# Performance work log

Measured on AMD Instinct MI355X. Metric: run time of the kernel, lower is better.

Reference implementation:

```python
import jax, jax.numpy as jnp
import numpy as np

B, S, D, H = 2, 2048, 2048, 16
DK = D // H


def setup_inputs() -> dict:
    key = jax.random.key(0)
    k1, k2, k3 = jax.random.split(key, 3)
    x = jax.random.normal(k1, (B, S, D), dtype=jnp.float32)
    # trunc-normal in the original; plain normal with matching std is fine for a numeric baseline
    std_qkv = 2.0 / (DK + D)  # note: original passes variance as std to trunc_normal_
    W_qkv = jax.random.normal(k2, (3 * D, D), dtype=jnp.float32) * std_qkv
    W_o = jax.random.normal(k3, (D, D), dtype=jnp.float32) * (1.0 / D)
    return {"x": x, "W_qkv": W_qkv, "W_o": W_o}


def reference(x, W_qkv, W_o):
    b, s, d = x.shape
    # fused QKV projection: y = x @ W_qkv^T
    qkv = jnp.einsum('bsd,ed->bse', x, W_qkv)  # [b, s, 3d]
    q, k, v = jnp.split(qkv, 3, axis=-1)
    # [b, s, d] -> [b, h, s, dk]
    def to_heads(t):
        return t.reshape(b, s, H, DK).transpose(0, 2, 1, 3)
    q, k, v = to_heads(q), to_heads(k), to_heads(v)
    scores = jnp.einsum('bhqd,bhkd->bhqk', q, k) / np.sqrt(DK).astype(np.float32)
    causal = jnp.tril(jnp.ones((s, s), dtype=bool))
    scores = jnp.where(causal, scores, -jnp.inf)
    att = jax.nn.softmax(scores, axis=-1)
    out = jnp.einsum('bhqk,bhkd->bhqd', att, v)  # [b, h, s, dk]
    out = out.transpose(0, 2, 1, 3).reshape(b, s, d)
    return jnp.einsum('bsd,od->bso', out, W_o)
```

## Files before the change

### kernel.cpp

```cpp
#include <hip/hip_runtime.h>

typedef _Float16 f16;
typedef _Float16 f16x4 __attribute__((ext_vector_type(4)));
typedef _Float16 f16x8 __attribute__((ext_vector_type(8)));
typedef float    f32x4 __attribute__((ext_vector_type(4)));

#define MFMA_F16(a,b,c) __builtin_amdgcn_mfma_f32_16x16x32_f16((a),(b),(c),0,0,0)

static constexpr int B_  = 2;
static constexpr int S_  = 2048;
static constexpr int D_  = 2048;
static constexpr int H_  = 16;
static constexpr int DK_ = 128;
static constexpr int K_  = 2048;

__device__ __forceinline__ void gload_lds16(const void* g, void* l) {
  __builtin_amdgcn_global_load_lds(
      (const __attribute__((address_space(1))) void*)g,
      (__attribute__((address_space(3))) void*)l, 16, 0, 0);
}

__global__ __launch_bounds__(256) void cast_f16_kernel(const float* __restrict__ in,
                                                       f16* __restrict__ out, int n4) {
  int i = blockIdx.x * 256 + threadIdx.x;
  int stride = gridDim.x * 256;
  for (int j = i; j < n4; j += stride) {
    float4 v = reinterpret_cast<const float4*>(in)[j];
    f16x4 o = {(f16)v.x, (f16)v.y, (f16)v.z, (f16)v.w};
    reinterpret_cast<f16x4*>(out)[j] = o;
  }
}

__device__ __forceinline__ void gemm_core(const f16* __restrict__ A, const f16* __restrict__ Bw,
                                          int brow, int bcol, f16* As, f16* Bs,
                                          f32x4 (&acc)[4][4]) {
  const int tid = threadIdx.x;
  const int w = tid >> 6, l = tid & 63;
  const int lg = l >> 4, lr = l & 15;
  const int wr = w >> 1, wc = w & 1;
#pragma unroll
  for (int mi = 0; mi < 4; ++mi)
#pragma unroll
    for (int ni = 0; ni < 4; ++ni) acc[mi][ni] = (f32x4){0.f, 0.f, 0.f, 0.f};

  const int rA = brow * 128 + (l >> 2);
  const int rB = bcol * 128 + (l >> 2);
  const int ck = (l & 3) * 8;

  for (int kt = 0; kt < K_ / 32; ++kt) {
    __syncthreads();
#pragma unroll
    for (int i = 0; i < 2; ++i) {
      const int c = w + i * 4;
      gload_lds16(A  + (size_t)(rA + c * 16) * K_ + kt * 32 + ck, As + c * 512);
      gload_lds16(Bw + (size_t)(rB + c * 16) * K_ + kt * 32 + ck, Bs + c * 512);
    }
    __syncthreads();
    f16x8 af[4], bf[4];
#pragma unroll
    for (int mi = 0; mi < 4; ++mi)
      af[mi] = *(const f16x8*)(As + (wr * 64 + mi * 16 + lr) * 32 + lg * 8);
#pragma unroll
    for (int ni = 0; ni < 4; ++ni)
      bf[ni] = *(const f16x8*)(Bs + (wc * 64 + ni * 16 + lr) * 32 + lg * 8);
#pragma unroll
    for (int mi = 0; mi < 4; ++mi)
#pragma unroll
      for (int ni = 0; ni < 4; ++ni)
        acc[mi][ni] = MFMA_F16(af[mi], bf[ni], acc[mi][ni]);
  }
}

__global__ __launch_bounds__(256) void gemm_qkv_kernel(const f16* __restrict__ xb,
                                                       const f16* __restrict__ wqkv,
                                                       f16* __restrict__ Q,
                                                       f16* __restrict__ Kk,
                                                       f16* __restrict__ V) {
  __shared__ __align__(16) f16 As[4096];
  __shared__ __align__(16) f16 Bs[4096];
  const int bid = blockIdx.x;
  const int swz = (bid & 7) * (1536 / 8) + (bid >> 3);
  const int brow = swz / 48, bcol = swz % 48;

  f32x4 acc[4][4];
  gemm_core(xb, wqkv, brow, bcol, As, Bs, acc);

  const int tid = threadIdx.x;
  const int w = tid >> 6, l = tid & 63;
  const int lg = l >> 4, lr = l & 15;
  const int wr = w >> 1, wc = w & 1;

  const int which = bcol / 16;
  const int h = bcol % 16;
  f16* outp = (which == 0) ? Q : ((which == 1) ? Kk : V);
  const float scale = (which == 0) ? 0.08838834764831845f : 1.0f;

#pragma unroll
  for (int mi = 0; mi < 4; ++mi) {
    const int mbase = brow * 128 + wr * 64 + mi * 16 + lg * 4;
#pragma unroll
    for (int ni = 0; ni < 4; ++ni) {
      const int dk = wc * 64 + ni * 16 + lr;
#pragma unroll
      for (int r = 0; r < 4; ++r) {
        const int mm = mbase + r;
        const int b = mm >> 11, s = mm & 2047;
        outp[(((size_t)b * H_ + h) * S_ + s) * DK_ + dk] = (f16)(acc[mi][ni][r] * scale);
      }
    }
  }
}

__global__ __launch_bounds__(256) void gemm_out_kernel(const f16* __restrict__ ab,
                                                       const f16* __restrict__ wo,
                                                       float* __restrict__ out) {
  __shared__ __align__(16) f16 As[4096];
  __shared__ __align__(16) f16 Bs[4096];
  const int bid = blockIdx.x;
  const int swz = (bid & 7) * (512 / 8) + (bid >> 3);
  const int brow = swz / 16, bcol = swz % 16;

  f32x4 acc[4][4];
  gemm_core(ab, wo, brow, bcol, As, Bs, acc);

  const int tid = threadIdx.x;
  const int w = tid >> 6, l = tid & 63;
  const int lg = l >> 4, lr = l & 15;
  const int wr = w >> 1, wc = w & 1;

#pragma unroll
  for (int mi = 0; mi < 4; ++mi) {
    const int mbase = brow * 128 + wr * 64 + mi * 16 + lg * 4;
#pragma unroll
    for (int ni = 0; ni < 4; ++ni) {
      const int n = bcol * 128 + wc * 64 + ni * 16 + lr;
#pragma unroll
      for (int r = 0; r < 4; ++r)
        out[(size_t)(mbase + r) * D_ + n] = acc[mi][ni][r];
    }
  }
}

__global__ __launch_bounds__(256) void transpose_v_kernel(const f16* __restrict__ V,
                                                          f16* __restrict__ Vt) {
  const int bid = blockIdx.x;
  const int dt = bid & 1;
  const int st = (bid >> 1) & 31;
  const int bh = bid >> 6;
  __shared__ __align__(16) f16 t[64][72];
  const int tid = threadIdx.x;
#pragma unroll
  for (int i = 0; i < 2; ++i) {
    const int chunk = i * 256 + tid;
    const int row = chunk >> 3, c8 = chunk & 7;
    f16x8 v = *(const f16x8*)(V + ((size_t)bh * S_ + st * 64 + row) * DK_ + dt * 64 + c8 * 8);
    *(f16x8*)&t[row][c8 * 8] = v;
  }
  __syncthreads();
#pragma unroll
  for (int i = 0; i < 2; ++i) {
    const int chunk = i * 256 + tid;
    const int row = chunk >> 3, c8 = chunk & 7;
    f16x8 v;
#pragma unroll
    for (int jj = 0; jj < 8; ++jj) v[jj] = t[c8 * 8 + jj][row];
    *(f16x8*)(Vt + ((size_t)bh * DK_ + dt * 64 + row) * S_ + st * 64 + c8 * 8) = v;
  }
}

__global__ __launch_bounds__(256) void attn_kernel(const f16* __restrict__ Q,
                                                   const f16* __restrict__ Kg,
                                                   const f16* __restrict__ Vt,
                                                   f16* __restrict__ O) {
  __shared__ __align__(16) unsigned char Ks[64 * 256];
  __shared__ __align__(16) unsigned char Vs[128 * 128];
  __shared__ __align__(16) unsigned char Ps[4][16 * 128];

  const int bid = blockIdx.x;
  const int pr = bid & 15;
  const int h  = (bid >> 4) & 15;
  const int b  = bid >> 8;
  const int bh = b * H_ + h;
  const int tid = threadIdx.x;
  const int w = tid >> 6, l = tid & 63;
  const int lg = l >> 4, lr = l & 15;

  for (int half = 0; half < 2; ++half) {
    const int qt = half ? (31 - pr) : pr;

    const f16* Qg = Q + ((size_t)bh * S_ + qt * 64 + w * 16) * DK_;
    f16x8 qf[4];
#pragma unroll
    for (int kd = 0; kd < 4; ++kd)
      qf[kd] = *(const f16x8*)(Qg + (size_t)lr * DK_ + kd * 32 + lg * 8);

    f32x4 o[8];
#pragma unroll
    for (int n = 0; n < 8; ++n) o[n] = (f32x4){0.f, 0.f, 0.f, 0.f};
    float mrun[4] = {-1e30f, -1e30f, -1e30f, -1e30f};
    float lrun[4] = {0.f, 0.f, 0.f, 0.f};

    const int ntiles = qt + 1;
    for (int kt = 0; kt < ntiles; ++kt) {
      __syncthreads();
      const f16* Kt = Kg + ((size_t)bh * S_ + kt * 64) * DK_;
#pragma unroll
      for (int i = 0; i < 4; ++i) {
        const int chunk = i * 256 + tid;
        const int row = chunk >> 4, c8 = chunk & 15;
        uint4 v = *(const uint4*)(Kt + (size_t)row * DK_ + c8 * 8);
        *(uint4*)(Ks + row * 256 + ((c8 * 16) ^ ((row & 7) << 4))) = v;
      }
      const f16* Vtt = Vt + (size_t)bh * DK_ * S_ + kt * 64;
#pragma unroll
      for (int i = 0; i < 4; ++i) {
        const int chunk = i * 256 + tid;
        const int row = chunk >> 3, c8 = chunk & 7;
        uint4 v = *(const uint4*)(Vtt + (size_t)row * S_ + c8 * 8);
        *(uint4*)(Vs + row * 128 + ((c8 * 16) ^ ((row & 7) << 4))) = v;
      }
      __syncthreads();

      f32x4 s[4];
#pragma unroll
      for (int j = 0; j < 4; ++j) s[j] = (f32x4){0.f, 0.f, 0.f, 0.f};
#pragma unroll
      for (int j = 0; j < 4; ++j) {
        const int row = j * 16 + lr;
#pragma unroll
        for (int kd = 0; kd < 4; ++kd) {
          f16x8 kf = *(const f16x8*)(Ks + row * 256 + ((kd * 64 + lg * 16) ^ ((row & 7) << 4)));
          s[j] = MFMA_F16(qf[kd], kf, s[j]);
        }
      }
      if (kt == qt) {
#pragma unroll
        for (int j = 0; j < 4; ++j) {
          const int col = j * 16 + lr;
#pragma unroll
          for (int r = 0; r < 4; ++r) {
            const int qrow = w * 16 + lg * 4 + r;
            if (col > qrow) s[j][r] = -1e30f;
          }
        }
      }
      float scl[4];
#pragma unroll
      for (int r = 0; r < 4; ++r) {
        float m0 = fmaxf(fmaxf(s[0][r], s[1][r]), fmaxf(s[2][r], s[3][r]));
#pragma unroll
        for (int msk = 1; msk < 16; msk <<= 1) m0 = fmaxf(m0, __shfl_xor(m0, msk, 64));
        const float nm = fmaxf(mrun[r], m0);
        scl[r] = __expf(mrun[r] - nm);
        mrun[r] = nm;
      }
      float rs[4] = {0.f, 0.f, 0.f, 0.f};
#pragma unroll
      for (int j = 0; j < 4; ++j) {
#pragma unroll
        for (int r = 0; r < 4; ++r) {
          const float p = __expf(fmaxf(s[j][r] - mrun[r], -80.f));
          rs[r] += p;
          const int row = lg * 4 + r;
          const int cb = (j * 16 + lr) * 2;
          *(f16*)(Ps[w] + row * 128 + (cb ^ ((row & 7) << 4))) = (f16)p;
        }
      }
#pragma unroll
      for (int r = 0; r < 4; ++r) {
        float t = rs[r];
#pragma unroll
        for (int msk = 1; msk < 16; msk <<= 1) t += __shfl_xor(t, msk, 64);
        lrun[r] = lrun[r] * scl[r] + t;
      }
#pragma unroll
      for (int n = 0; n < 8; ++n)
#pragma unroll
        for (int r = 0; r < 4; ++r) o[n][r] *= scl[r];

      asm volatile("s_waitcnt lgkmcnt(0)" ::: "memory");

#pragma unroll
      for (int ks = 0; ks < 2; ++ks) {
        f16x8 pf = *(const f16x8*)(Ps[w] + lr * 128 + ((ks * 64 + lg * 16) ^ ((lr & 7) << 4)));
#pragma unroll
        for (int n = 0; n < 8; ++n) {
          const int row = n * 16 + lr;
          f16x8 vf = *(const f16x8*)(Vs + row * 128 + ((ks * 64 + lg * 16) ^ ((row & 7) << 4)));
          o[n] = MFMA_F16(pf, vf, o[n]);
        }
      }
    }

#pragma unroll
    for (int r = 0; r < 4; ++r) {
      const float inv = 1.0f / lrun[r];
      const int srow = qt * 64 + w * 16 + lg * 4 + r;
      f16* op = O + ((size_t)b * S_ + srow) * D_ + h * DK_;
#pragma unroll
      for (int n = 0; n < 8; ++n) op[n * 16 + lr] = (f16)(o[n][r] * inv);
    }
  }
}

extern "C" void kernel_launch(void* const* d_in, const int* in_sizes, int n_in,
                              void* d_out, int out_size, void* d_ws, size_t ws_size,
                              hipStream_t stream) {
  const float* x    = (const float*)d_in[0];
  const float* wqkv = (const float*)d_in[1];
  const float* wo   = (const float*)d_in[2];
  float* out = (float*)d_out;
  char* ws = (char*)d_ws;

  f16* xb     = (f16*)(ws + 0);
  f16* wqkvb  = (f16*)(ws + 16777216);
  f16* wob    = (f16*)(ws + 41943040);
  f16* Qb     = (f16*)(ws + 50331648);
  f16* Kb     = (f16*)(ws + 67108864);
  f16* Vb     = (f16*)(ws + 83886080);
  f16* Vtb    = (f16*)(ws + 16777216);
  f16* attn_o = (f16*)(ws + 0);

  cast_f16_kernel<<<2048, 256, 0, stream>>>(x, xb, 8388608 / 4);
  cast_f16_kernel<<<2048, 256, 0, stream>>>(wqkv, wqkvb, 12582912 / 4);
  cast_f16_kernel<<<1024, 256, 0, stream>>>(wo, wob, 4194304 / 4);

  gemm_qkv_kernel<<<1536, 256, 0, stream>>>(xb, wqkvb, Qb, Kb, Vb);
  transpose_v_kernel<<<2048, 256, 0, stream>>>(Vb, Vtb);
  attn_kernel<<<512, 256, 0, stream>>>(Qb, Kb, Vtb, attn_o);
  gemm_out_kernel<<<512, 256, 0, stream>>>(attn_o, wob, out);
}
```

Measured before the change: 305.1 us.

## Pipeline GEMM K-loop with a 4-stage LDS ring buffer of async loads

```diff
diff --git a/kernel.cpp b/kernel.cpp
--- a/kernel.cpp
+++ b/kernel.cpp
@@ -13,6 +13,7 @@
 static constexpr int H_  = 16;
 static constexpr int DK_ = 128;
 static constexpr int K_  = 2048;
+static constexpr int NKT = K_ / 32;
 
 __device__ __forceinline__ void gload_lds16(const void* g, void* l) {
   __builtin_amdgcn_global_load_lds(
@@ -31,59 +32,92 @@
   }
 }
 
-__device__ __forceinline__ void gemm_core(const f16* __restrict__ A, const f16* __restrict__ Bw,
-                                          int brow, int bcol, f16* As, f16* Bs,
+
+__device__ __forceinline__ void ring_stage(const f16* gA0, const f16* gA1,
+                                           const f16* gB0, const f16* gB1,
+                                           int tt, char* lds, int w) {
+  char* base = lds + (tt & 3) * 16384;
+  gload_lds16(gA0 + tt * 32, base +         w * 1024);
+  gload_lds16(gA1 + tt * 32, base +  4096 + w * 1024);
+  gload_lds16(gB0 + tt * 32, base +  8192 + w * 1024);
+  gload_lds16(gB1 + tt * 32, base + 12288 + w * 1024);
+}
+
+__device__ __forceinline__ void ring_step(const char* base, int wr, int wc, int lr, int lg,
                                           f32x4 (&acc)[4][4]) {
+  f16x8 af[4], bf[4];
+#pragma unroll
+  for (int mi = 0; mi < 4; ++mi)
+    af[mi] = *(const f16x8*)(base + (wr * 4 + mi) * 1024 + (lr * 4 + lg) * 16);
+#pragma unroll
+  for (int ni = 0; ni < 4; ++ni)
+    bf[ni] = *(const f16x8*)(base + 8192 + (wc * 4 + ni) * 1024 + (lr * 4 + lg) * 16);
+#pragma unroll
+  for (int mi = 0; mi < 4; ++mi)
+#pragma unroll
+    for (int ni = 0; ni < 4; ++ni)
+      acc[mi][ni] = MFMA_F16(af[mi], bf[ni], acc[mi][ni]);
+}
+
+#define RING_SYNC(N)                                          \
+  asm volatile("s_waitcnt vmcnt(" #N ")" ::: "memory");       \
+  __builtin_amdgcn_s_barrier();                               \
+  asm volatile("" ::: "memory");
+
+__device__ __forceinline__ void gemm_core_ring(const f16* __restrict__ A,
+                                               const f16* __restrict__ Bw,
+                                               int brow, int bcol, char* lds,
+                                               f32x4 (&acc)[4][4]) {
   const int tid = threadIdx.x;
   const int w = tid >> 6, l = tid & 63;
   const int lg = l >> 4, lr = l & 15;
   const int wr = w >> 1, wc = w & 1;
+  const int srow = l >> 2;
+  const int scol = (l & 3) * 8;
+
 #pragma unroll
   for (int mi = 0; mi < 4; ++mi)
 #pragma unroll
     for (int ni = 0; ni < 4; ++ni) acc[mi][ni] = (f32x4){0.f, 0.f, 0.f, 0.f};
 
-  const int rA = brow * 128 + (l >> 2);
-  const int rB = bcol * 128 + (l >> 2);
-  const int ck = (l & 3) * 8;
-
-  for (int kt = 0; kt < K_ / 32; ++kt) {
-    __syncthreads();
-#pragma unroll
-    for (int i = 0; i < 2; ++i) {
-      const int c = w + i * 4;
-      gload_lds16(A  + (size_t)(rA + c * 16) * K_ + kt * 32 + ck, As + c * 512);
-      gload_lds16(Bw + (size_t)(rB + c * 16) * K_ + kt * 32 + ck, Bs + c * 512);
-    }
-    __syncthreads();
-    f16x8 af[4], bf[4];
-#pragma unroll
-    for (int mi = 0; mi < 4; ++mi)
-      af[mi] = *(const f16x8*)(As + (wr * 64 + mi * 16 + lr) * 32 + lg * 8);
-#pragma unroll
-    for (int ni = 0; ni < 4; ++ni)
-      bf[ni] = *(const f16x8*)(Bs + (wc * 64 + ni * 16 + lr) * 32 + lg * 8);
-#pragma unroll
-    for (int mi = 0; mi < 4; ++mi)
-#pragma unroll
-      for (int ni = 0; ni < 4; ++ni)
-        acc[mi][ni] = MFMA_F16(af[mi], bf[ni], acc[mi][ni]);
-  }
-}
-
-__global__ __launch_bounds__(256) void gemm_qkv_kernel(const f16* __restrict__ xb,
-                                                       const f16* __restrict__ wqkv,
-                                                       f16* __restrict__ Q,
-                                                       f16* __restrict__ Kk,
-                                                       f16* __restrict__ V) {
-  __shared__ __align__(16) f16 As[4096];
-  __shared__ __align__(16) f16 Bs[4096];
+  const f16* gA0 = A  + (size_t)(brow * 128 + w * 16 + srow) * K_ + scol;
+  const f16* gA1 = gA0 + (size_t)64 * K_;
+  const f16* gB0 = Bw + (size_t)(bcol * 128 + w * 16 + srow) * K_ + scol;
+  const f16* gB1 = gB0 + (size_t)64 * K_;
+
+  ring_stage(gA0, gA1, gB0, gB1, 0, lds, w);
+  ring_stage(gA0, gA1, gB0, gB1, 1, lds, w);
+  ring_stage(gA0, gA1, gB0, gB1, 2, lds, w);
+  RING_SYNC(8)
+
+#pragma unroll 4
+  for (int t = 0; t < NKT - 4; ++t) {
+    ring_stage(gA0, gA1, gB0, gB1, t + 3, lds, w);
+    ring_step(lds + (t & 3) * 16384, wr, wc, lr, lg, acc);
+    RING_SYNC(8)
+  }
+  ring_stage(gA0, gA1, gB0, gB1, NKT - 1, lds, w);
+  ring_step(lds + ((NKT - 4) & 3) * 16384, wr, wc, lr, lg, acc);
+  RING_SYNC(8)
+  ring_step(lds + ((NKT - 3) & 3) * 16384, wr, wc, lr, lg, acc);
+  RING_SYNC(4)
+  ring_step(lds + ((NKT - 2) & 3) * 16384, wr, wc, lr, lg, acc);
+  RING_SYNC(0)
+  ring_step(lds + ((NKT - 1) & 3) * 16384, wr, wc, lr, lg, acc);
+}
+
+__global__ __launch_bounds__(256, 2) void gemm_qkv_kernel(const f16* __restrict__ xb,
+                                                          const f16* __restrict__ wqkv,
+                                                          f16* __restrict__ Q,
+                                                          f16* __restrict__ Kk,
+                                                          f16* __restrict__ V) {
+  __shared__ __align__(16) char lds[65536];
   const int bid = blockIdx.x;
-  const int swz = (bid & 7) * (1536 / 8) + (bid >> 3);
+  const int swz = (bid & 7) * 192 + (bid >> 3);
   const int brow = swz / 48, bcol = swz % 48;
 
   f32x4 acc[4][4];
-  gemm_core(xb, wqkv, brow, bcol, As, Bs, acc);
+  gemm_core_ring(xb, wqkv, brow, bcol, lds, acc);
 
   const int tid = threadIdx.x;
   const int w = tid >> 6, l = tid & 63;
@@ -111,17 +145,16 @@
   }
 }
 
-__global__ __launch_bounds__(256) void gemm_out_kernel(const f16* __restrict__ ab,
-                                                       const f16* __restrict__ wo,
-                                                       float* __restrict__ out) {
-  __shared__ __align__(16) f16 As[4096];
-  __shared__ __align__(16) f16 Bs[4096];
+__global__ __launch_bounds__(256, 2) void gemm_out_kernel(const f16* __restrict__ ab,
+                                                          const f16* __restrict__ wo,
+                                                          float* __restrict__ out) {
+  __shared__ __align__(16) char lds[65536];
   const int bid = blockIdx.x;
-  const int swz = (bid & 7) * (512 / 8) + (bid >> 3);
+  const int swz = (bid & 7) * 64 + (bid >> 3);
   const int brow = swz / 16, bcol = swz % 16;
 
   f32x4 acc[4][4];
-  gemm_core(ab, wo, brow, bcol, As, Bs, acc);
+  gemm_core_ring(ab, wo, brow, bcol, lds, acc);
 
   const int tid = threadIdx.x;
   const int w = tid >> 6, l = tid & 63;
```

After: 311.4 us. 1.02x slower.
